# Performance work log

Measured on AMD Instinct MI355X. Metric: run time of the kernel, lower is better.

Reference implementation:

```python
import jax, jax.numpy as jnp
import numpy as np

T, B, F = 128, 128, 1024
ALPHA_BASE, LAMBDA_BASE = 0.97, 0.95
THETA_BASE, BETA_THETA = 0.1, 0.01
RHO, GATE_ALPHA = 0.25, 5.0        # gate_cfg rho_B/rho_C, alpha
NUDGE, PHASE_SCALE = 0.1, 0.02     # gate_cfg additive_nudge, ei_cfg phase_corr_scale
MIX_AMP, MIX_NOV, MIX_INST = 1.0, 0.5, 0.5


def _adaptive_percentile_threshold(score, rho, alpha):
    # keep top-rho fraction per row: tau = (1-rho)-quantile, soft sigmoid gate
    tau = jnp.quantile(score, 1.0 - rho, axis=-1, keepdims=True)
    return jax.nn.sigmoid(alpha * (score - tau)), tau


def setup_inputs() -> dict:
    key = jax.random.key(0)
    k0, k1, k2, k3 = jax.random.split(key, 4)
    return {
        "in_re": jax.random.normal(k0, (T, B, F), jnp.float32),
        "in_im": jax.random.normal(k1, (T, B, F), jnp.float32),
        "r_re": 0.05 * jax.random.normal(k2, (F,), jnp.float32),
        "r_im": 0.05 * jax.random.normal(k3, (F,), jnp.float32),
        "alpha_map": jnp.zeros((F,), jnp.float32),
        "lambda_map": jnp.zeros((F,), jnp.float32),
    }


def reference(in_re, in_im, r_re, r_im, alpha_map, lambda_map):
    sg = jax.lax.stop_gradient
    alpha = jnp.clip(ALPHA_BASE + 0.05 * jnp.tanh(alpha_map), 0.9, 0.995)  # [F]
    lam = jnp.clip(LAMBDA_BASE + 0.05 * jnp.tanh(lambda_map), 0.9, 0.995)  # [F]
    r_conj = jnp.conj(r_re + 1j * r_im)                                    # [F] c64
    theta_base = jnp.full((F,), THETA_BASE, jnp.float32)
    in_field = (in_re + 1j * in_im).astype(jnp.complex64)                  # [T,B,F]

    carry0 = dict(
        X=jnp.zeros((B, F), jnp.complex64),
        sA=jnp.zeros((B, F), jnp.float32),
        sB=jnp.zeros((B, F), jnp.float32),
        sC=jnp.zeros((B, F), jnp.float32),
        theta=theta_base,
        mu=jnp.zeros((F,), jnp.float32),
        var=jnp.full((F,), 0.01, jnp.float32),
        ema_unit=jnp.zeros((F,), jnp.complex64),
        b_usage=jnp.zeros((F,), jnp.float32),
        c_usage=jnp.zeros((F,), jnp.float32),
    )

    def step(c, u):
        X_mid = alpha * c["X"] + u                       # [B,F] c64
        amp = jnp.abs(X_mid)
        unit = jnp.exp(1j * jnp.angle(X_mid))            # unit phase
        # EMA stats (torch.no_grad -> stop_gradient)
        mu = sg(0.9 * c["mu"] + 0.1 * amp.mean(0))
        var = sg(0.9 * c["var"] + 0.1 * ((amp - mu[None]) ** 2).mean(0))
        ema_unit = sg(0.9 * c["ema_unit"] + 0.1 * unit.mean(0))
        plv = jnp.abs(ema_unit)                          # [F]
        zscore = (amp - mu[None]) / (jnp.sqrt(var)[None] + 1e-3)
        instab = (1.0 - plv)[None]
        score = MIX_AMP * amp + MIX_NOV * jnp.abs(zscore) + MIX_INST * instab
        gB, _ = _adaptive_percentile_threshold(score, RHO, GATE_ALPHA)
        gC, _ = _adaptive_percentile_threshold(-score, RHO, GATE_ALPHA)
        XB = X_mid * gB
        XC = X_mid * gC
        sA = lam * c["sA"] + jnp.real(X_mid * r_conj)
        sB = lam * c["sB"] + jnp.real(XB * r_conj)
        sC = lam * c["sC"] + jnp.real(XC * r_conj)
        evA = (sA >= c["theta"]).astype(jnp.float32)
        evB = (sB >= c["theta"]).astype(jnp.float32)
        evC = (sC >= c["theta"]).astype(jnp.float32)
        # threshold homeostasis (no_grad)
        theta = c["theta"] + 0.01 * evB.mean(0) - 0.01 * evC.mean(0)
        theta = jnp.clip(theta - BETA_THETA * (theta - theta_base), 0.01, 10.0)
        # reentry_mode='full': phase correction + additive nudge
        corr = (evB.mean(0) > 0).astype(jnp.float32)[None]  # [1,F]
        XA = X_mid * jnp.exp(1j * PHASE_SCALE * corr)
        XA = XA + NUDGE * (XB * corr)
        b_usage = 0.99 * c["b_usage"] + 0.01 * evB.mean(0)
        c_usage = 0.99 * c["c_usage"] + 0.01 * evC.mean(0)
        new = dict(X=XA, sA=sA, sB=sB, sC=sC, theta=theta, mu=mu, var=var,
                   ema_unit=ema_unit, b_usage=b_usage, c_usage=c_usage)
        return new, sA

    _, sA_seq = jax.lax.scan(step, carry0, in_field)
    return sA_seq  # [T,B,F]
```

## Files before the change

kernel.cpp:

```cpp
#include <hip/hip_runtime.h>
#include <math.h>


#define T_STEPS 128
#define B_DIM   128
#define F_DIM   1024
#define NWG     128
#define NTH     256
#define BF      (B_DIM * F_DIM)

typedef unsigned long long ull;

__device__ __forceinline__ ull ld64(const ull* p) {
  return __hip_atomic_load(p, __ATOMIC_RELAXED, __HIP_MEMORY_SCOPE_AGENT);
}
__device__ __forceinline__ void st64(ull* p, ull v) {
  __hip_atomic_store(p, v, __ATOMIC_RELAXED, __HIP_MEMORY_SCOPE_AGENT);
}

extern "C" __global__ void __launch_bounds__(NTH)
ResonatorABC_82094004896068_kernel(
    const float* __restrict__ in_re, const float* __restrict__ in_im,
    const float* __restrict__ r_re_p, const float* __restrict__ r_im_p,
    const float* __restrict__ alpha_map, const float* __restrict__ lambda_map,
    float* __restrict__ out, ull* __restrict__ ws)
{
  const int tid  = threadIdx.x;
  const int wg   = blockIdx.x;
  const int fl   = tid & 7;
  const int rg   = tid >> 3;
  const int f    = (wg << 3) + fl;
  const int wid  = tid >> 6;
  const int lane = tid & 63;

  ull* score64 = ws;
  ull* taubox  = ws + BF;

  __shared__ __align__(16) float pamp[4][8][4];
  __shared__ __align__(16) float pfin[8][4];
  __shared__ __align__(16) float pev[4][8][2];
  __shared__ __align__(16) float evfin[8][2];
  __shared__ __align__(16) unsigned h[1024];
  __shared__ unsigned wsum[4];
  __shared__ unsigned mmw[4][2];
  __shared__ unsigned tbin[4], tbase[4], tcnt[4];
  __shared__ unsigned lcnt[4];
  __shared__ unsigned lists[4][256];
  __shared__ unsigned resv[4], resf[4];
  __shared__ unsigned rmm[2];
  __shared__ unsigned t2[3];
  __shared__ float tauLds[256];

  const float af = fminf(fmaxf(0.97f + 0.05f * tanhf(alpha_map[f]), 0.90f), 0.995f);
  const float lf = fminf(fmaxf(0.95f + 0.05f * tanhf(lambda_map[f]), 0.90f), 0.995f);
  const float rr = r_re_p[f];
  const float ri = r_im_p[f];
  const float c002 = cosf(0.02f);
  const float s002 = sinf(0.02f);

  float X_re[4] = {0.f,0.f,0.f,0.f}, X_im[4] = {0.f,0.f,0.f,0.f};
  float sA[4] = {0.f,0.f,0.f,0.f}, sB[4] = {0.f,0.f,0.f,0.f}, sC[4] = {0.f,0.f,0.f,0.f};
  float mu = 0.f, var = 0.01f, theta = 0.1f, ema_re = 0.f, ema_im = 0.f;

  int idx[4];
  float ur[4], ui[4];
  #pragma unroll
  for (int k = 0; k < 4; ++k) {
    idx[k] = (rg + 32 * k) * F_DIM + f;
    ur[k] = in_re[idx[k]];
    ui[k] = in_im[idx[k]];
  }

  const unsigned KR[4] = {255u, 256u, 767u, 768u};

  for (int t = 0; t < T_STEPS; ++t) {
    const ull want = (ull)(t + 1);

    *(uint4*)&h[4 * tid] = make_uint4(0u, 0u, 0u, 0u);

    float Xm_re[4], Xm_im[4], proj[4], amp[4], score[4];
    float a0 = 0.f, a1 = 0.f, a2 = 0.f, a3 = 0.f;
    #pragma unroll
    for (int k = 0; k < 4; ++k) {
      Xm_re[k] = af * X_re[k] + ur[k];
      Xm_im[k] = af * X_im[k] + ui[k];
      float amp2 = Xm_re[k] * Xm_re[k] + Xm_im[k] * Xm_im[k];
      amp[k] = sqrtf(amp2);
      float invamp = (amp[k] > 0.f) ? (1.0f / amp[k]) : 0.f;
      float un_re = (amp[k] > 0.f) ? (Xm_re[k] * invamp) : 1.0f;
      float un_im = Xm_im[k] * invamp;
      proj[k] = Xm_re[k] * rr + Xm_im[k] * ri;
      sA[k] = lf * sA[k] + proj[k];
      out[t * BF + idx[k]] = sA[k];
      a0 += amp[k]; a1 += amp2; a2 += un_re; a3 += un_im;
    }
    #pragma unroll
    for (int m = 8; m < 64; m <<= 1) {
      a0 += __shfl_xor(a0, m);
      a1 += __shfl_xor(a1, m);
      a2 += __shfl_xor(a2, m);
      a3 += __shfl_xor(a3, m);
    }
    if (lane < 8) { *(float4*)&pamp[wid][lane][0] = make_float4(a0, a1, a2, a3); }
    __syncthreads();
    if (tid < 32) {
      int sfl = tid >> 2, q = tid & 3;
      pfin[sfl][q] = pamp[0][sfl][q] + pamp[1][sfl][q] + pamp[2][sfl][q] + pamp[3][sfl][q];
    }
    __syncthreads();
    float4 SS = *(const float4*)&pfin[fl][0];
    float m1 = SS.x * 0.0078125f;
    float m2 = SS.y * 0.0078125f;
    mu = 0.9f * mu + 0.1f * m1;
    float vm = m2 - 2.f * mu * m1 + mu * mu;
    vm = fmaxf(vm, 0.f);
    var = 0.9f * var + 0.1f * vm;
    ema_re = 0.9f * ema_re + 0.1f * (SS.z * 0.0078125f);
    ema_im = 0.9f * ema_im + 0.1f * (SS.w * 0.0078125f);
    float plv = sqrtf(ema_re * ema_re + ema_im * ema_im);
    float sden = sqrtf(var) + 1e-3f;
    #pragma unroll
    for (int k = 0; k < 4; ++k) {
      float zs = (amp[k] - mu) / sden;
      score[k] = amp[k] + 0.5f * fabsf(zs) + 0.5f * (1.0f - plv);
      st64(&score64[idx[k]], (want << 32) | (ull)__float_as_uint(score[k]));
    }

    float ur_n[4] = {0.f,0.f,0.f,0.f}, ui_n[4] = {0.f,0.f,0.f,0.f};
    if (t + 1 < T_STEPS) {
      #pragma unroll
      for (int k = 0; k < 4; ++k) {
        ur_n[k] = in_re[(t + 1) * BF + idx[k]];
        ui_n[k] = in_im[(t + 1) * BF + idx[k]];
      }
    }

    unsigned uval[4], bin[4];
    {
      const ull* sp0 = &score64[wg * F_DIM + tid];
      ull v[4]; bool ok[4] = {false, false, false, false};
      int remaining = 4;
      while (remaining) {
        #pragma unroll
        for (int k = 0; k < 4; ++k) if (!ok[k]) v[k] = ld64(sp0 + 256 * k);
        #pragma unroll
        for (int k = 0; k < 4; ++k) {
          if (!ok[k] && (v[k] >> 32) == want) { ok[k] = true; uval[k] = (unsigned)v[k]; --remaining; }
        }
        if (remaining) __builtin_amdgcn_s_sleep(1);
      }
    }
    unsigned umin = min(min(uval[0], uval[1]), min(uval[2], uval[3]));
    unsigned umax = max(max(uval[0], uval[1]), max(uval[2], uval[3]));
    #pragma unroll
    for (int m = 1; m < 64; m <<= 1) {
      umin = min(umin, (unsigned)__shfl_xor((int)umin, m));
      umax = max(umax, (unsigned)__shfl_xor((int)umax, m));
    }
    if (lane == 0) { mmw[wid][0] = umin; mmw[wid][1] = umax; }
    __syncthreads();
    unsigned lo = min(min(mmw[0][0], mmw[1][0]), min(mmw[2][0], mmw[3][0]));
    unsigned hi = max(max(mmw[0][1], mmw[1][1]), max(mmw[2][1], mmw[3][1]));

    if (lo != hi) {
      ull rng = (ull)hi - (ull)lo + 1ull;
      ull inv = (1ull << 40) / rng;
      #pragma unroll
      for (int k = 0; k < 4; ++k) {
        bin[k] = (unsigned)((((ull)(uval[k] - lo)) * inv) >> 30);
        atomicAdd(&h[bin[k]], 1u);
      }
      if (tid < 4) { lcnt[tid] = 0u; resf[tid] = 0u; }
      __syncthreads();
      uint4 hc = *(const uint4*)&h[4 * tid];
      unsigned s4 = hc.x + hc.y + hc.z + hc.w;
      unsigned incl = s4;
      #pragma unroll
      for (int d = 1; d < 64; d <<= 1) {
        unsigned vv = __shfl_up(incl, d);
        if (lane >= d) incl += vv;
      }
      if (lane == 63) wsum[wid] = incl;
      __syncthreads();
      unsigned woff = 0u;
      for (int w = 0; w < 4; ++w) if (w < wid) woff += wsum[w];
      unsigned gexcl = woff + incl - s4;
      unsigned cv[4] = {hc.x, hc.y, hc.z, hc.w};
      unsigned bb[4];
      bb[0] = gexcl; bb[1] = bb[0] + cv[0]; bb[2] = bb[1] + cv[1]; bb[3] = bb[2] + cv[2];
      #pragma unroll
      for (int i = 0; i < 4; ++i) {
        if (cv[i] > 0u) {
          #pragma unroll
          for (int r = 0; r < 4; ++r) {
            if (bb[i] <= KR[r] && KR[r] < bb[i] + cv[i]) {
              tbin[r] = 4 * tid + i; tbase[r] = bb[i]; tcnt[r] = cv[i];
            }
          }
        }
      }
      __syncthreads();
      unsigned b0 = tbin[0], b1 = tbin[1], b2 = tbin[2], b3 = tbin[3];
      #pragma unroll
      for (int k = 0; k < 4; ++k) {
        unsigned bk = bin[k], uv = uval[k];
        if (bk == b0) { unsigned s = atomicAdd(&lcnt[0], 1u); if (s < 256u) lists[0][s] = uv; }
        else if (bk == b1 && b1 != b0) { unsigned s = atomicAdd(&lcnt[1], 1u); if (s < 256u) lists[1][s] = uv; }
        else if (bk == b2 && b2 != b1) { unsigned s = atomicAdd(&lcnt[2], 1u); if (s < 256u) lists[2][s] = uv; }
        else if (bk == b3 && b3 != b2) { unsigned s = atomicAdd(&lcnt[3], 1u); if (s < 256u) lists[3][s] = uv; }
      }
      __syncthreads();
      {
        const int j = wid;
        int src = j;
        while (src > 0 && tbin[src - 1] == tbin[j]) --src;
        unsigned c = tcnt[j];
        if (c <= 256u) {
          unsigned kk = KR[j] - tbase[j];
          for (int bi = 0; bi < (int)c; bi += 64) {
            int i = bi + lane;
            if (i < (int)c) {
              unsigned e = lists[src][i];
              unsigned r = 0;
              for (int q = 0; q < (int)c; ++q) {
                unsigned x = lists[src][q];
                r += (x < e || (x == e && q < i)) ? 1u : 0u;
              }
              if (r == kk) { resv[j] = e; resf[j] = 1u; }
            }
          }
        }
      }
      __syncthreads();
      for (int j = 0; j < 4; ++j) {
        if (resf[j]) continue;
        bool inj[4];
        #pragma unroll
        for (int k = 0; k < 4; ++k) inj[k] = (bin[k] == tbin[j]);
        unsigned krem = KR[j] - tbase[j];
        for (int iter = 0; iter < 40; ++iter) {
          if (tid == 0) { rmm[0] = 0xFFFFFFFFu; rmm[1] = 0u; }
          __syncthreads();
          #pragma unroll
          for (int k = 0; k < 4; ++k)
            if (inj[k]) { atomicMin(&rmm[0], uval[k]); atomicMax(&rmm[1], uval[k]); }
          __syncthreads();
          unsigned wlo = rmm[0], whi = rmm[1];
          if (wlo == whi) { if (tid == 0) { resv[j] = wlo; resf[j] = 1u; } __syncthreads(); break; }
          *(uint4*)&h[4 * tid] = make_uint4(0u, 0u, 0u, 0u);
          __syncthreads();
          ull rng2 = (ull)whi - (ull)wlo + 1ull;
          ull inv2 = (1ull << 40) / rng2;
          unsigned nb[4];
          #pragma unroll
          for (int k = 0; k < 4; ++k) {
            nb[k] = inj[k] ? (unsigned)((((ull)(uval[k] - wlo)) * inv2) >> 30) : 0u;
            if (inj[k]) atomicAdd(&h[nb[k]], 1u);
          }
          __syncthreads();
          uint4 hc2 = *(const uint4*)&h[4 * tid];
          unsigned s42 = hc2.x + hc2.y + hc2.z + hc2.w;
          unsigned incl2 = s42;
          #pragma unroll
          for (int d = 1; d < 64; d <<= 1) {
            unsigned vv = __shfl_up(incl2, d);
            if (lane >= d) incl2 += vv;
          }
          if (lane == 63) wsum[wid] = incl2;
          if (tid == 0) lcnt[0] = 0u;
          __syncthreads();
          unsigned woff2 = 0u;
          for (int w = 0; w < 4; ++w) if (w < wid) woff2 += wsum[w];
          unsigned gexcl2 = woff2 + incl2 - s42;
          unsigned cv2[4] = {hc2.x, hc2.y, hc2.z, hc2.w};
          unsigned bb2[4];
          bb2[0] = gexcl2; bb2[1] = bb2[0] + cv2[0]; bb2[2] = bb2[1] + cv2[1]; bb2[3] = bb2[2] + cv2[2];
          #pragma unroll
          for (int i = 0; i < 4; ++i) {
            if (cv2[i] > 0u && bb2[i] <= krem && krem < bb2[i] + cv2[i]) {
              t2[0] = 4 * tid + i; t2[1] = bb2[i]; t2[2] = cv2[i];
            }
          }
          __syncthreads();
          unsigned nbin = t2[0], nbase = t2[1], ncnt = t2[2];
          bool newin[4];
          #pragma unroll
          for (int k = 0; k < 4; ++k) newin[k] = inj[k] && (nb[k] == nbin);
          if (ncnt <= 256u) {
            #pragma unroll
            for (int k = 0; k < 4; ++k)
              if (newin[k]) { unsigned s = atomicAdd(&lcnt[0], 1u); if (s < 256u) lists[0][s] = uval[k]; }
            __syncthreads();
            if (wid == 0) {
              unsigned kk2 = krem - nbase;
              for (int bi = 0; bi < (int)ncnt; bi += 64) {
                int i = bi + lane;
                if (i < (int)ncnt) {
                  unsigned e = lists[0][i];
                  unsigned r = 0;
                  for (int q = 0; q < (int)ncnt; ++q) {
                    unsigned x = lists[0][q];
                    r += (x < e || (x == e && q < i)) ? 1u : 0u;
                  }
                  if (r == kk2) { resv[j] = e; resf[j] = 1u; }
                }
              }
            }
            __syncthreads();
            break;
          }
          #pragma unroll
          for (int k = 0; k < 4; ++k) inj[k] = newin[k];
          krem -= nbase;
        }
      }
    } else {
      if (tid < 4) { resv[tid] = lo; resf[tid] = 1u; }
      __syncthreads();
    }

    {
      float s255 = __uint_as_float(resv[0]);
      float s256 = __uint_as_float(resv[1]);
      float s767 = __uint_as_float(resv[2]);
      float s768 = __uint_as_float(resv[3]);
      float tb = 0.75f * s767 + 0.25f * s768;
      float tc = -(0.75f * s256 + 0.25f * s255);
      int c = tid & 127;
      ull w = (tid < 128)
            ? ((want << 32) | (ull)__float_as_uint(tb))
            : ((want << 32) | (ull)__float_as_uint(tc));
      int slot = (tid < 128) ? wg : (128 + wg);
      st64(&taubox[(ull)c * 256 + slot], w);
    }

    {
      const ull* src = &taubox[(ull)wg * 256 + tid];
      ull v2 = ld64(src);
      while ((v2 >> 32) != want) { __builtin_amdgcn_s_sleep(1); v2 = ld64(src); }
      tauLds[tid] = __uint_as_float((unsigned)v2);
    }
    __syncthreads();

    float gB[4];
    float e0 = 0.f, e1 = 0.f;
    #pragma unroll
    for (int k = 0; k < 4; ++k) {
      float tb = tauLds[rg + 32 * k];
      float tc = tauLds[128 + rg + 32 * k];
      float sc = score[k];
      gB[k] = 1.0f / (1.0f + expf(-5.0f * (sc - tb)));
      float gC = 1.0f / (1.0f + expf(-5.0f * (-sc - tc)));
      sB[k] = lf * sB[k] + proj[k] * gB[k];
      sC[k] = lf * sC[k] + proj[k] * gC;
      e0 += (sB[k] >= theta) ? 1.0f : 0.0f;
      e1 += (sC[k] >= theta) ? 1.0f : 0.0f;
    }
    #pragma unroll
    for (int m = 8; m < 64; m <<= 1) {
      e0 += __shfl_xor(e0, m);
      e1 += __shfl_xor(e1, m);
    }
    if (lane < 8) { pev[wid][lane][0] = e0; pev[wid][lane][1] = e1; }
    __syncthreads();
    if (tid < 16) {
      int sfl = tid >> 1, q = tid & 1;
      evfin[sfl][q] = pev[0][sfl][q] + pev[1][sfl][q] + pev[2][sfl][q] + pev[3][sfl][q];
    }
    __syncthreads();
    float cB = evfin[fl][0];
    float cC = evfin[fl][1];
    float th1 = theta + 0.01f * (cB * 0.0078125f) - 0.01f * (cC * 0.0078125f);
    theta = fminf(fmaxf(th1 - 0.01f * (th1 - 0.1f), 0.01f), 10.0f);
    bool corr = (cB > 0.f);
    #pragma unroll
    for (int k = 0; k < 4; ++k) {
      float fac_re = corr ? (c002 + 0.1f * gB[k]) : 1.0f;
      float fac_im = corr ? s002 : 0.0f;
      X_re[k] = Xm_re[k] * fac_re - Xm_im[k] * fac_im;
      X_im[k] = Xm_re[k] * fac_im + Xm_im[k] * fac_re;
      ur[k] = ur_n[k]; ui[k] = ui_n[k];
    }
  }
}

extern "C" void kernel_launch(void* const* d_in, const int* in_sizes, int n_in,
                              void* d_out, int out_size, void* d_ws, size_t ws_size,
                              hipStream_t stream) {
  const float* in_re = (const float*)d_in[0];
  const float* in_im = (const float*)d_in[1];
  const float* r_re  = (const float*)d_in[2];
  const float* r_im  = (const float*)d_in[3];
  const float* amap  = (const float*)d_in[4];
  const float* lmap  = (const float*)d_in[5];
  float* out = (float*)d_out;
  ull* ws = (ull*)d_ws;
  hipMemsetAsync(d_ws, 0, (size_t)(BF + 128 * 256) * 8, stream);
  hipLaunchKernelGGL(ResonatorABC_82094004896068_kernel,
                     dim3(NWG), dim3(NTH), 0, stream,
                     in_re, in_im, r_re, r_im, amap, lmap, out, ws);
}
```

Before: 1.203 ms.

## Use adaptive predicted histogram window for quantile selection, drop min/max reduction

Replaces the per-step block-wide min/max reduction with a persistent value window carried across timesteps, binning scores by a power-of-two shift with clamping instead of a 64-bit divide. The bin scan moves to a single wavefront of 16 bins per lane, which also derives the next step's window from the occupied bins. It removes redundant LDS reduction passes and their barriers for the mean and event sums, and changes the spin-wait sleep intervals. Clamped outlier bins at the window edges may force the refinement loop to run more often when the window prediction is poor.

After: 1.314 ms. 1.09x slower.

```diff
diff --git a/kernel.cpp b/kernel.cpp
--- a/kernel.cpp
+++ b/kernel.cpp
@@ -37,12 +37,10 @@
   ull* taubox  = ws + BF;
 
   __shared__ __align__(16) float pamp[4][8][4];
-  __shared__ __align__(16) float pfin[8][4];
   __shared__ __align__(16) float pev[4][8][2];
-  __shared__ __align__(16) float evfin[8][2];
   __shared__ __align__(16) unsigned h[1024];
   __shared__ unsigned wsum[4];
-  __shared__ unsigned mmw[4][2];
+  __shared__ unsigned win[2];
   __shared__ unsigned tbin[4], tbase[4], tcnt[4];
   __shared__ unsigned lcnt[4];
   __shared__ unsigned lists[4][256];
@@ -72,6 +70,9 @@
   }
 
   const unsigned KR[4] = {255u, 256u, 767u, 768u};
+
+  if (tid == 0) { win[0] = 0x3E000000u; win[1] = 0x42000000u; }
+  __syncthreads();
 
   for (int t = 0; t < T_STEPS; ++t) {
     const ull want = (ull)(t + 1);
@@ -103,20 +104,22 @@
     }
     if (lane < 8) { *(float4*)&pamp[wid][lane][0] = make_float4(a0, a1, a2, a3); }
     __syncthreads();
-    if (tid < 32) {
-      int sfl = tid >> 2, q = tid & 3;
-      pfin[sfl][q] = pamp[0][sfl][q] + pamp[1][sfl][q] + pamp[2][sfl][q] + pamp[3][sfl][q];
-    }
-    __syncthreads();
-    float4 SS = *(const float4*)&pfin[fl][0];
-    float m1 = SS.x * 0.0078125f;
-    float m2 = SS.y * 0.0078125f;
+    float4 P0 = *(const float4*)&pamp[0][fl][0];
+    float4 P1 = *(const float4*)&pamp[1][fl][0];
+    float4 P2 = *(const float4*)&pamp[2][fl][0];
+    float4 P3 = *(const float4*)&pamp[3][fl][0];
+    float S0 = P0.x + P1.x + P2.x + P3.x;
+    float S1 = P0.y + P1.y + P2.y + P3.y;
+    float S2 = P0.z + P1.z + P2.z + P3.z;
+    float S3 = P0.w + P1.w + P2.w + P3.w;
+    float m1 = S0 * 0.0078125f;
+    float m2 = S1 * 0.0078125f;
     mu = 0.9f * mu + 0.1f * m1;
     float vm = m2 - 2.f * mu * m1 + mu * mu;
     vm = fmaxf(vm, 0.f);
     var = 0.9f * var + 0.1f * vm;
-    ema_re = 0.9f * ema_re + 0.1f * (SS.z * 0.0078125f);
-    ema_im = 0.9f * ema_im + 0.1f * (SS.w * 0.0078125f);
+    ema_re = 0.9f * ema_re + 0.1f * (S2 * 0.0078125f);
+    ema_im = 0.9f * ema_im + 0.1f * (S3 * 0.0078125f);
     float plv = sqrtf(ema_re * ema_re + ema_im * ema_im);
     float sden = sqrtf(var) + 1e-3f;
     #pragma unroll
@@ -134,6 +137,12 @@
         ui_n[k] = in_im[(t + 1) * BF + idx[k]];
       }
     }
+
+    const unsigned wlo = win[0], whi = win[1];
+    const unsigned range = whi - wlo + 1u;
+    int shift = (range <= 1024u) ? 0 : (22 - __clz(range - 1u));
+    if (shift < 0) shift = 0;
+    const unsigned maxbin = (range - 1u) >> shift;
 
     unsigned uval[4], bin[4];
     {
@@ -147,59 +156,80 @@
         for (int k = 0; k < 4; ++k) {
           if (!ok[k] && (v[k] >> 32) == want) { ok[k] = true; uval[k] = (unsigned)v[k]; --remaining; }
         }
-        if (remaining) __builtin_amdgcn_s_sleep(1);
-      }
-    }
-    unsigned umin = min(min(uval[0], uval[1]), min(uval[2], uval[3]));
-    unsigned umax = max(max(uval[0], uval[1]), max(uval[2], uval[3]));
-    #pragma unroll
-    for (int m = 1; m < 64; m <<= 1) {
-      umin = min(umin, (unsigned)__shfl_xor((int)umin, m));
-      umax = max(umax, (unsigned)__shfl_xor((int)umax, m));
-    }
-    if (lane == 0) { mmw[wid][0] = umin; mmw[wid][1] = umax; }
-    __syncthreads();
-    unsigned lo = min(min(mmw[0][0], mmw[1][0]), min(mmw[2][0], mmw[3][0]));
-    unsigned hi = max(max(mmw[0][1], mmw[1][1]), max(mmw[2][1], mmw[3][1]));
-
-    if (lo != hi) {
-      ull rng = (ull)hi - (ull)lo + 1ull;
-      ull inv = (1ull << 40) / rng;
-      #pragma unroll
-      for (int k = 0; k < 4; ++k) {
-        bin[k] = (unsigned)((((ull)(uval[k] - lo)) * inv) >> 30);
-        atomicAdd(&h[bin[k]], 1u);
-      }
-      if (tid < 4) { lcnt[tid] = 0u; resf[tid] = 0u; }
-      __syncthreads();
-      uint4 hc = *(const uint4*)&h[4 * tid];
-      unsigned s4 = hc.x + hc.y + hc.z + hc.w;
-      unsigned incl = s4;
+        if (remaining) __builtin_amdgcn_s_sleep(4);
+      }
+    }
+    #pragma unroll
+    for (int k = 0; k < 4; ++k) {
+      unsigned uc = min(max(uval[k], wlo), whi);
+      bin[k] = (uc - wlo) >> shift;
+      atomicAdd(&h[bin[k]], 1u);
+    }
+    if (tid >= 64 && tid < 68) { lcnt[tid - 64] = 0u; resf[tid - 64] = 0u; }
+    __syncthreads();
+
+    if (wid == 0) {
+      uint4 q0 = *(const uint4*)&h[16 * lane +  0];
+      uint4 q1 = *(const uint4*)&h[16 * lane +  4];
+      uint4 q2 = *(const uint4*)&h[16 * lane +  8];
+      uint4 q3 = *(const uint4*)&h[16 * lane + 12];
+      unsigned c16[16] = {q0.x,q0.y,q0.z,q0.w, q1.x,q1.y,q1.z,q1.w,
+                          q2.x,q2.y,q2.z,q2.w, q3.x,q3.y,q3.z,q3.w};
+      unsigned s16 = 0;
+      #pragma unroll
+      for (int i = 0; i < 16; ++i) s16 += c16[i];
+      unsigned incl = s16;
       #pragma unroll
       for (int d = 1; d < 64; d <<= 1) {
         unsigned vv = __shfl_up(incl, d);
         if (lane >= d) incl += vv;
       }
-      if (lane == 63) wsum[wid] = incl;
-      __syncthreads();
-      unsigned woff = 0u;
-      for (int w = 0; w < 4; ++w) if (w < wid) woff += wsum[w];
-      unsigned gexcl = woff + incl - s4;
-      unsigned cv[4] = {hc.x, hc.y, hc.z, hc.w};
-      unsigned bb[4];
-      bb[0] = gexcl; bb[1] = bb[0] + cv[0]; bb[2] = bb[1] + cv[1]; bb[3] = bb[2] + cv[2];
-      #pragma unroll
-      for (int i = 0; i < 4; ++i) {
-        if (cv[i] > 0u) {
+      unsigned excl = incl - s16;
+      unsigned bacc = excl;
+      #pragma unroll
+      for (int i = 0; i < 16; ++i) {
+        unsigned c = c16[i];
+        if (c) {
           #pragma unroll
           for (int r = 0; r < 4; ++r) {
-            if (bb[i] <= KR[r] && KR[r] < bb[i] + cv[i]) {
-              tbin[r] = 4 * tid + i; tbase[r] = bb[i]; tcnt[r] = cv[i];
+            if (bacc <= KR[r] && KR[r] < bacc + c) {
+              tbin[r] = 16 * lane + i; tbase[r] = bacc; tcnt[r] = c;
             }
           }
         }
-      }
-      __syncthreads();
+        bacc += c;
+      }
+      int fi = 16, li = -1;
+      #pragma unroll
+      for (int i = 0; i < 16; ++i) if (c16[i]) { if (fi == 16) fi = i; li = i; }
+      unsigned long long occ = __ballot(s16 > 0);
+      int flane = __builtin_ctzll(occ);
+      int llane = 63 - __builtin_clzll(occ);
+      int fin = __shfl(fi, flane);
+      int lin = __shfl(li, llane);
+      if (lane == 0) {
+        unsigned first_bin = (unsigned)(16 * flane + fin);
+        unsigned last_bin  = (unsigned)(16 * llane + lin);
+        unsigned nlo, nhi;
+        if (first_bin == 0u) {
+          unsigned w4 = range >> 2;
+          nlo = (wlo > w4) ? (wlo - w4) : 0u;
+        } else {
+          nlo = wlo + ((first_bin - 1u) << shift);
+        }
+        if (last_bin >= maxbin) {
+          ull tt = (ull)whi + (ull)(range >> 2);
+          nhi = (tt > 0x7F7FFFFFull) ? 0x7F7FFFFFu : (unsigned)tt;
+        } else {
+          ull tt = (ull)wlo + (((ull)(last_bin + 2u)) << shift) - 1ull;
+          nhi = (tt > 0x7F7FFFFFull) ? 0x7F7FFFFFu : (unsigned)tt;
+        }
+        win[0] = nlo; win[1] = nhi;
+      }
+    }
+    __syncthreads();
+
+    {
       unsigned b0 = tbin[0], b1 = tbin[1], b2 = tbin[2], b3 = tbin[3];
       #pragma unroll
       for (int k = 0; k < 4; ++k) {
@@ -209,114 +239,113 @@
         else if (bk == b2 && b2 != b1) { unsigned s = atomicAdd(&lcnt[2], 1u); if (s < 256u) lists[2][s] = uv; }
         else if (bk == b3 && b3 != b2) { unsigned s = atomicAdd(&lcnt[3], 1u); if (s < 256u) lists[3][s] = uv; }
       }
-      __syncthreads();
-      {
-        const int j = wid;
-        int src = j;
-        while (src > 0 && tbin[src - 1] == tbin[j]) --src;
-        unsigned c = tcnt[j];
-        if (c <= 256u) {
-          unsigned kk = KR[j] - tbase[j];
-          for (int bi = 0; bi < (int)c; bi += 64) {
-            int i = bi + lane;
-            if (i < (int)c) {
-              unsigned e = lists[src][i];
-              unsigned r = 0;
-              for (int q = 0; q < (int)c; ++q) {
-                unsigned x = lists[src][q];
-                r += (x < e || (x == e && q < i)) ? 1u : 0u;
-              }
-              if (r == kk) { resv[j] = e; resf[j] = 1u; }
+    }
+    __syncthreads();
+
+    {
+      const int j = wid;
+      int src = j;
+      while (src > 0 && tbin[src - 1] == tbin[j]) --src;
+      unsigned c = tcnt[j];
+      if (c <= 256u) {
+        unsigned kk = KR[j] - tbase[j];
+        for (int bi = 0; bi < (int)c; bi += 64) {
+          int i = bi + lane;
+          if (i < (int)c) {
+            unsigned e = lists[src][i];
+            unsigned r = 0;
+            for (int q = 0; q < (int)c; ++q) {
+              unsigned x = lists[src][q];
+              r += (x < e || (x == e && q < i)) ? 1u : 0u;
             }
+            if (r == kk) { resv[j] = e; resf[j] = 1u; }
           }
         }
       }
-      __syncthreads();
-      for (int j = 0; j < 4; ++j) {
-        if (resf[j]) continue;
-        bool inj[4];
-        #pragma unroll
-        for (int k = 0; k < 4; ++k) inj[k] = (bin[k] == tbin[j]);
-        unsigned krem = KR[j] - tbase[j];
-        for (int iter = 0; iter < 40; ++iter) {
-          if (tid == 0) { rmm[0] = 0xFFFFFFFFu; rmm[1] = 0u; }
-          __syncthreads();
+    }
+    __syncthreads();
+
+    for (int j = 0; j < 4; ++j) {
+      if (resf[j]) continue;
+      bool inj[4];
+      #pragma unroll
+      for (int k = 0; k < 4; ++k) inj[k] = (bin[k] == tbin[j]);
+      unsigned krem = KR[j] - tbase[j];
+      for (int iter = 0; iter < 40; ++iter) {
+        if (tid == 0) { rmm[0] = 0xFFFFFFFFu; rmm[1] = 0u; }
+        __syncthreads();
+        #pragma unroll
+        for (int k = 0; k < 4; ++k)
+          if (inj[k]) { atomicMin(&rmm[0], uval[k]); atomicMax(&rmm[1], uval[k]); }
+        __syncthreads();
+        unsigned wlo2 = rmm[0], whi2 = rmm[1];
+        if (wlo2 == whi2) { if (tid == 0) { resv[j] = wlo2; resf[j] = 1u; } __syncthreads(); break; }
+        *(uint4*)&h[4 * tid] = make_uint4(0u, 0u, 0u, 0u);
+        __syncthreads();
+        ull rng2 = (ull)whi2 - (ull)wlo2 + 1ull;
+        ull inv2 = (1ull << 40) / rng2;
+        unsigned nb[4];
+        #pragma unroll
+        for (int k = 0; k < 4; ++k) {
+          nb[k] = inj[k] ? (unsigned)((((ull)(uval[k] - wlo2)) * inv2) >> 30) : 0u;
+          if (inj[k]) atomicAdd(&h[nb[k]], 1u);
+        }
+        __syncthreads();
+        uint4 hc2 = *(const uint4*)&h[4 * tid];
+        unsigned s42 = hc2.x + hc2.y + hc2.z + hc2.w;
+        unsigned incl2 = s42;
+        #pragma unroll
+        for (int d = 1; d < 64; d <<= 1) {
+          unsigned vv = __shfl_up(incl2, d);
+          if (lane >= d) incl2 += vv;
+        }
+        if (lane == 63) wsum[wid] = incl2;
+        if (tid == 0) lcnt[0] = 0u;
+        __syncthreads();
+        unsigned woff2 = 0u;
+        for (int w = 0; w < 4; ++w) if (w < wid) woff2 += wsum[w];
+        unsigned gexcl2 = woff2 + incl2 - s42;
+        unsigned cv2[4] = {hc2.x, hc2.y, hc2.z, hc2.w};
+        unsigned bb2[4];
+        bb2[0] = gexcl2; bb2[1] = bb2[0] + cv2[0]; bb2[2] = bb2[1] + cv2[1]; bb2[3] = bb2[2] + cv2[2];
+        #pragma unroll
+        for (int i = 0; i < 4; ++i) {
+          if (cv2[i] > 0u && bb2[i] <= krem && krem < bb2[i] + cv2[i]) {
+            t2[0] = 4 * tid + i; t2[1] = bb2[i]; t2[2] = cv2[i];
+          }
+        }
+        __syncthreads();
+        unsigned nbin = t2[0], nbase = t2[1], ncnt = t2[2];
+        bool newin[4];
+        #pragma unroll
+        for (int k = 0; k < 4; ++k) newin[k] = inj[k] && (nb[k] == nbin);
+        if (ncnt <= 256u) {
           #pragma unroll
           for (int k = 0; k < 4; ++k)
-            if (inj[k]) { atomicMin(&rmm[0], uval[k]); atomicMax(&rmm[1], uval[k]); }
+            if (newin[k]) { unsigned s = atomicAdd(&lcnt[0], 1u); if (s < 256u) lists[0][s] = uval[k]; }
           __syncthreads();
-          unsigned wlo = rmm[0], whi = rmm[1];
-          if (wlo == whi) { if (tid == 0) { resv[j] = wlo; resf[j] = 1u; } __syncthreads(); break; }
-          *(uint4*)&h[4 * tid] = make_uint4(0u, 0u, 0u, 0u);
-          __syncthreads();
-          ull rng2 = (ull)whi - (ull)wlo + 1ull;
-          ull inv2 = (1ull << 40) / rng2;
-          unsigned nb[4];
-          #pragma unroll
-          for (int k = 0; k < 4; ++k) {
-            nb[k] = inj[k] ? (unsigned)((((ull)(uval[k] - wlo)) * inv2) >> 30) : 0u;
-            if (inj[k]) atomicAdd(&h[nb[k]], 1u);
-          }
-          __syncthreads();
-          uint4 hc2 = *(const uint4*)&h[4 * tid];
-          unsigned s42 = hc2.x + hc2.y + hc2.z + hc2.w;
-          unsigned incl2 = s42;
-          #pragma unroll
-          for (int d = 1; d < 64; d <<= 1) {
-            unsigned vv = __shfl_up(incl2, d);
-            if (lane >= d) incl2 += vv;
-          }
-          if (lane == 63) wsum[wid] = incl2;
-          if (tid == 0) lcnt[0] = 0u;
-          __syncthreads();
-          unsigned woff2 = 0u;
-          for (int w = 0; w < 4; ++w) if (w < wid) woff2 += wsum[w];
-          unsigned gexcl2 = woff2 + incl2 - s42;
-          unsigned cv2[4] = {hc2.x, hc2.y, hc2.z, hc2.w};
-          unsigned bb2[4];
-          bb2[0] = gexcl2; bb2[1] = bb2[0] + cv2[0]; bb2[2] = bb2[1] + cv2[1]; bb2[3] = bb2[2] + cv2[2];
-          #pragma unroll
-          for (int i = 0; i < 4; ++i) {
-            if (cv2[i] > 0u && bb2[i] <= krem && krem < bb2[i] + cv2[i]) {
-              t2[0] = 4 * tid + i; t2[1] = bb2[i]; t2[2] = cv2[i];
+          if (wid == 0) {
+            unsigned kk2 = krem - nbase;
+            for (int bi = 0; bi < (int)ncnt; bi += 64) {
+              int i = bi + lane;
+              if (i < (int)ncnt) {
+                unsigned e = lists[0][i];
+                unsigned r = 0;
+                for (int q = 0; q < (int)ncnt; ++q) {
+                  unsigned x = lists[0][q];
+                  r += (x < e || (x == e && q < i)) ? 1u : 0u;
+                }
+                if (r == kk2) { resv[j] = e; resf[j] = 1u; }
+              }
             }
           }
           __syncthreads();
-          unsigned nbin = t2[0], nbase = t2[1], ncnt = t2[2];
-          bool newin[4];
-          #pragma unroll
-          for (int k = 0; k < 4; ++k) newin[k] = inj[k] && (nb[k] == nbin);
-          if (ncnt <= 256u) {
-            #pragma unroll
-            for (int k = 0; k < 4; ++k)
-              if (newin[k]) { unsigned s = atomicAdd(&lcnt[0], 1u); if (s < 256u) lists[0][s] = uval[k]; }
-            __syncthreads();
-            if (wid == 0) {
-              unsigned kk2 = krem - nbase;
-              for (int bi = 0; bi < (int)ncnt; bi += 64) {
-                int i = bi + lane;
-                if (i < (int)ncnt) {
-                  unsigned e = lists[0][i];
-                  unsigned r = 0;
-                  for (int q = 0; q < (int)ncnt; ++q) {
-                    unsigned x = lists[0][q];
-                    r += (x < e || (x == e && q < i)) ? 1u : 0u;
-                  }
-                  if (r == kk2) { resv[j] = e; resf[j] = 1u; }
-                }
-              }
-            }
-            __syncthreads();
-            break;
-          }
-          #pragma unroll
-          for (int k = 0; k < 4; ++k) inj[k] = newin[k];
-          krem -= nbase;
-        }
-      }
-    } else {
-      if (tid < 4) { resv[tid] = lo; resf[tid] = 1u; }
-      __syncthreads();
+          break;
+        }
+        #pragma unroll
+        for (int k = 0; k < 4; ++k) inj[k] = newin[k];
+        krem -= nbase;
+      }
     }
 
     {
@@ -337,7 +366,7 @@
     {
       const ull* src = &taubox[(ull)wg * 256 + tid];
       ull v2 = ld64(src);
-      while ((v2 >> 32) != want) { __builtin_amdgcn_s_sleep(1); v2 = ld64(src); }
+      while ((v2 >> 32) != want) { __builtin_amdgcn_s_sleep(2); v2 = ld64(src); }
       tauLds[tid] = __uint_as_float((unsigned)v2);
     }
     __syncthreads();
@@ -363,13 +392,12 @@
     }
     if (lane < 8) { pev[wid][lane][0] = e0; pev[wid][lane][1] = e1; }
     __syncthreads();
-    if (tid < 16) {
-      int sfl = tid >> 1, q = tid & 1;
-      evfin[sfl][q] = pev[0][sfl][q] + pev[1][sfl][q] + pev[2][sfl][q] + pev[3][sfl][q];
-    }
-    __syncthreads();
-    float cB = evfin[fl][0];
-    float cC = evfin[fl][1];
+    float2 E0 = *(const float2*)&pev[0][fl][0];
+    float2 E1 = *(const float2*)&pev[1][fl][0];
+    float2 E2 = *(const float2*)&pev[2][fl][0];
+    float2 E3 = *(const float2*)&pev[3][fl][0];
+    float cB = E0.x + E1.x + E2.x + E3.x;
+    float cC = E0.y + E1.y + E2.y + E3.y;
     float th1 = theta + 0.01f * (cB * 0.0078125f) - 0.01f * (cC * 0.0078125f);
     theta = fminf(fmaxf(th1 - 0.01f * (th1 - 0.1f), 0.01f), 10.0f);
     bool corr = (cB > 0.f);
```

## Pack cross-workgroup exchange tags into 32-bit parity words and compact tau mailbox

Applied to the files above, without the earlier changes.

Scores and per-row thresholds shared between workgroups are now stored as 32-bit words, with a parity bit in the sign position as the step tag, instead of 64-bit value/step-counter pairs. This halves the global traffic of the per-step score exchange. The tau mailbox shrinks from a 128x256 scatter, where every thread wrote a slot, to two 128-entry arrays written by one thread per workgroup and read by all. The goal is to cut memory traffic and atomic-store volume on the per-step cross-workgroup synchronization path. It relies on scores being non-negative so the sign bit is free, and on step ordering preventing a writer from running two steps ahead of a reader.

New measurement: 1.282 ms. +6.6%, slower.

```diff
diff --git a/kernel.cpp b/kernel.cpp
--- a/kernel.cpp
+++ b/kernel.cpp
@@ -11,10 +11,10 @@
 
 typedef unsigned long long ull;
 
-__device__ __forceinline__ ull ld64(const ull* p) {
+__device__ __forceinline__ unsigned ld32(const unsigned* p) {
   return __hip_atomic_load(p, __ATOMIC_RELAXED, __HIP_MEMORY_SCOPE_AGENT);
 }
-__device__ __forceinline__ void st64(ull* p, ull v) {
+__device__ __forceinline__ void st32(unsigned* p, unsigned v) {
   __hip_atomic_store(p, v, __ATOMIC_RELAXED, __HIP_MEMORY_SCOPE_AGENT);
 }
 
@@ -23,7 +23,7 @@
     const float* __restrict__ in_re, const float* __restrict__ in_im,
     const float* __restrict__ r_re_p, const float* __restrict__ r_im_p,
     const float* __restrict__ alpha_map, const float* __restrict__ lambda_map,
-    float* __restrict__ out, ull* __restrict__ ws)
+    float* __restrict__ out, unsigned* __restrict__ ws)
 {
   const int tid  = threadIdx.x;
   const int wg   = blockIdx.x;
@@ -33,8 +33,9 @@
   const int wid  = tid >> 6;
   const int lane = tid & 63;
 
-  ull* score64 = ws;
-  ull* taubox  = ws + BF;
+  unsigned* score32 = ws;
+  unsigned* tauB32  = ws + BF;
+  unsigned* tauC32  = ws + BF + 128;
 
   __shared__ __align__(16) float pamp[4][8][4];
   __shared__ __align__(16) float pfin[8][4];
@@ -74,7 +75,8 @@
   const unsigned KR[4] = {255u, 256u, 767u, 768u};
 
   for (int t = 0; t < T_STEPS; ++t) {
-    const ull want = (ull)(t + 1);
+    const unsigned par = (unsigned)((t + 1) & 1);
+    const unsigned tagbit = par << 31;
 
     *(uint4*)&h[4 * tid] = make_uint4(0u, 0u, 0u, 0u);
 
@@ -123,7 +125,7 @@
     for (int k = 0; k < 4; ++k) {
       float zs = (amp[k] - mu) / sden;
       score[k] = amp[k] + 0.5f * fabsf(zs) + 0.5f * (1.0f - plv);
-      st64(&score64[idx[k]], (want << 32) | (ull)__float_as_uint(score[k]));
+      st32(&score32[idx[k]], __float_as_uint(score[k]) | tagbit);
     }
 
     float ur_n[4] = {0.f,0.f,0.f,0.f}, ui_n[4] = {0.f,0.f,0.f,0.f};
@@ -137,15 +139,15 @@
 
     unsigned uval[4], bin[4];
     {
-      const ull* sp0 = &score64[wg * F_DIM + tid];
-      ull v[4]; bool ok[4] = {false, false, false, false};
+      const unsigned* sp0 = &score32[wg * F_DIM + tid];
+      unsigned v[4]; bool ok[4] = {false, false, false, false};
       int remaining = 4;
       while (remaining) {
         #pragma unroll
-        for (int k = 0; k < 4; ++k) if (!ok[k]) v[k] = ld64(sp0 + 256 * k);
+        for (int k = 0; k < 4; ++k) if (!ok[k]) v[k] = ld32(sp0 + 256 * k);
         #pragma unroll
         for (int k = 0; k < 4; ++k) {
-          if (!ok[k] && (v[k] >> 32) == want) { ok[k] = true; uval[k] = (unsigned)v[k]; --remaining; }
+          if (!ok[k] && (v[k] >> 31) == par) { ok[k] = true; uval[k] = v[k] & 0x7FFFFFFFu; --remaining; }
         }
         if (remaining) __builtin_amdgcn_s_sleep(1);
       }
@@ -158,6 +160,7 @@
       umax = max(umax, (unsigned)__shfl_xor((int)umax, m));
     }
     if (lane == 0) { mmw[wid][0] = umin; mmw[wid][1] = umax; }
+    if (tid < 4) { lcnt[tid] = 0u; resf[tid] = 0u; }
     __syncthreads();
     unsigned lo = min(min(mmw[0][0], mmw[1][0]), min(mmw[2][0], mmw[3][0]));
     unsigned hi = max(max(mmw[0][1], mmw[1][1]), max(mmw[2][1], mmw[3][1]));
@@ -170,7 +173,6 @@
         bin[k] = (unsigned)((((ull)(uval[k] - lo)) * inv) >> 30);
         atomicAdd(&h[bin[k]], 1u);
       }
-      if (tid < 4) { lcnt[tid] = 0u; resf[tid] = 0u; }
       __syncthreads();
       uint4 hc = *(const uint4*)&h[4 * tid];
       unsigned s4 = hc.x + hc.y + hc.z + hc.w;
@@ -200,14 +202,16 @@
         }
       }
       __syncthreads();
-      unsigned b0 = tbin[0], b1 = tbin[1], b2 = tbin[2], b3 = tbin[3];
-      #pragma unroll
-      for (int k = 0; k < 4; ++k) {
-        unsigned bk = bin[k], uv = uval[k];
-        if (bk == b0) { unsigned s = atomicAdd(&lcnt[0], 1u); if (s < 256u) lists[0][s] = uv; }
-        else if (bk == b1 && b1 != b0) { unsigned s = atomicAdd(&lcnt[1], 1u); if (s < 256u) lists[1][s] = uv; }
-        else if (bk == b2 && b2 != b1) { unsigned s = atomicAdd(&lcnt[2], 1u); if (s < 256u) lists[2][s] = uv; }
-        else if (bk == b3 && b3 != b2) { unsigned s = atomicAdd(&lcnt[3], 1u); if (s < 256u) lists[3][s] = uv; }
+      {
+        unsigned b0 = tbin[0], b1 = tbin[1], b2 = tbin[2], b3 = tbin[3];
+        #pragma unroll
+        for (int k = 0; k < 4; ++k) {
+          unsigned bk = bin[k], uv = uval[k];
+          if (bk == b0) { unsigned s = atomicAdd(&lcnt[0], 1u); if (s < 256u) lists[0][s] = uv; }
+          else if (bk == b1 && b1 != b0) { unsigned s = atomicAdd(&lcnt[1], 1u); if (s < 256u) lists[1][s] = uv; }
+          else if (bk == b2 && b2 != b1) { unsigned s = atomicAdd(&lcnt[2], 1u); if (s < 256u) lists[2][s] = uv; }
+          else if (bk == b3 && b3 != b2) { unsigned s = atomicAdd(&lcnt[3], 1u); if (s < 256u) lists[3][s] = uv; }
+        }
       }
       __syncthreads();
       {
@@ -319,26 +323,22 @@
       __syncthreads();
     }
 
-    {
+    if (tid == 0) {
       float s255 = __uint_as_float(resv[0]);
       float s256 = __uint_as_float(resv[1]);
       float s767 = __uint_as_float(resv[2]);
       float s768 = __uint_as_float(resv[3]);
-      float tb = 0.75f * s767 + 0.25f * s768;
-      float tc = -(0.75f * s256 + 0.25f * s255);
-      int c = tid & 127;
-      ull w = (tid < 128)
-            ? ((want << 32) | (ull)__float_as_uint(tb))
-            : ((want << 32) | (ull)__float_as_uint(tc));
-      int slot = (tid < 128) ? wg : (128 + wg);
-      st64(&taubox[(ull)c * 256 + slot], w);
+      float tbq = 0.75f * s767 + 0.25f * s768;
+      float tcq = 0.75f * s256 + 0.25f * s255;
+      st32(&tauB32[wg], __float_as_uint(tbq) | tagbit);
+      st32(&tauC32[wg], __float_as_uint(tcq) | tagbit);
     }
 
     {
-      const ull* src = &taubox[(ull)wg * 256 + tid];
-      ull v2 = ld64(src);
-      while ((v2 >> 32) != want) { __builtin_amdgcn_s_sleep(1); v2 = ld64(src); }
-      tauLds[tid] = __uint_as_float((unsigned)v2);
+      const unsigned* src = (tid < 128) ? &tauB32[tid] : &tauC32[tid - 128];
+      unsigned v2 = ld32(src);
+      while ((v2 >> 31) != par) { __builtin_amdgcn_s_sleep(1); v2 = ld32(src); }
+      tauLds[tid] = __uint_as_float(v2 & 0x7FFFFFFFu);
     }
     __syncthreads();
 
@@ -347,10 +347,10 @@
     #pragma unroll
     for (int k = 0; k < 4; ++k) {
       float tb = tauLds[rg + 32 * k];
-      float tc = tauLds[128 + rg + 32 * k];
+      float q  = tauLds[128 + rg + 32 * k];
       float sc = score[k];
       gB[k] = 1.0f / (1.0f + expf(-5.0f * (sc - tb)));
-      float gC = 1.0f / (1.0f + expf(-5.0f * (-sc - tc)));
+      float gC = 1.0f / (1.0f + expf(-5.0f * (q - sc)));
       sB[k] = lf * sB[k] + proj[k] * gB[k];
       sC[k] = lf * sC[k] + proj[k] * gC;
       e0 += (sB[k] >= theta) ? 1.0f : 0.0f;
@@ -394,8 +394,8 @@
   const float* amap  = (const float*)d_in[4];
   const float* lmap  = (const float*)d_in[5];
   float* out = (float*)d_out;
-  ull* ws = (ull*)d_ws;
-  hipMemsetAsync(d_ws, 0, (size_t)(BF + 128 * 256) * 8, stream);
+  unsigned* ws = (unsigned*)d_ws;
+  hipMemsetAsync(d_ws, 0, (size_t)(BF + 256) * 4, stream);
   hipLaunchKernelGGL(ResonatorABC_82094004896068_kernel,
                      dim3(NWG), dim3(NTH), 0, stream,
                      in_re, in_im, r_re, r_im, amap, lmap, out, ws);
```
